# Kernel optimization log

Measured on AMD Instinct MI355X. Metric: run time of the kernel, lower is better.

The kernel has to match this reference:

```python
import jax, jax.numpy as jnp
import numpy as np

# hyperparameters (from init_kwargs)
GAMMA = 2.0
KEEP_WEIGHT = 1.0
T_TEMP = 0.07
M = 0.5
COS_M = float(np.cos(M))
SIN_M = float(np.sin(M))
THRESHOLD = float(np.cos(np.pi - M))
MM = float(np.sin(np.pi - M) * M)
ALPHA = 0.1
T_BUF0 = 0.0  # registered buffer t initialized to zero
VALID_THRESHOLD = 0.8
EPS = 1e-12  # F.normalize eps


def setup_inputs() -> dict:
    key = jax.random.key(0)
    k1, k2, k3 = jax.random.split(key, 3)
    N, C = 8192, 128
    return {
        "feature1": jax.random.normal(k1, (N, C), jnp.float32),
        "feature2": jax.random.normal(k2, (N, C), jnp.float32),
        "labels": jax.random.randint(k3, (N,), 0, 1024, dtype=jnp.int32),
    }


def reference(feature1, feature2, labels):
    N = feature1.shape[0]
    f1 = feature1 / jnp.maximum(jnp.linalg.norm(feature1, axis=1, keepdims=True), EPS)
    f2 = feature2 / jnp.maximum(jnp.linalg.norm(feature2, axis=1, keepdims=True), EPS)

    # [N, N] similarity, clamped to [-1, 1]
    sim = jnp.clip(jnp.einsum('nc,kc->nk', f1, f2), -1.0, 1.0)

    pos = (labels[:, None] == labels[None, :]).astype(sim.dtype)  # [N, N]
    neg = 1.0 - pos
    pos_mask = pos > 0

    # buffer update t (no_grad in original)
    mean_ts = jax.lax.stop_gradient((sim * pos).sum() / pos.sum())
    t = ALPHA * mean_ts + (1.0 - ALPHA) * T_BUF0
    weight_valid = t > VALID_THRESHOLD

    # curricular margin on positive entries
    sin_theta = jnp.sqrt(1.0 - sim * sim)
    cos_theta_m = sim * COS_M - sin_theta * SIN_M
    final_pos = jnp.where(sim > THRESHOLD, cos_theta_m, sim - MM)
    sim2 = jnp.where(pos_mask, final_pos, sim)

    # per-row mean of (margined) positive similarities
    row_target = (sim2 * pos).sum(axis=1) / pos.sum(axis=1)  # [N]
    hard_mask = sim2 > row_target[:, None]
    sim3 = jnp.where(hard_mask, sim2 * (t + sim2), sim2)
    sim4 = jnp.where(pos_mask, final_pos, sim3)

    logits = jnp.exp(sim4 / T_TEMP)

    # focal-style reweighting (only used when weight_valid)
    diff_pos = (pos - sim * pos) ** GAMMA + KEEP_WEIGHT * pos
    diff_neg = jnp.clip(sim * neg, 0.0, 1.0) ** GAMMA + KEEP_WEIGHT * neg

    logit_pos = jnp.where(weight_valid, (logits * diff_pos).sum(axis=1), (logits * pos).sum(axis=1))
    logit_neg = jnp.where(weight_valid, (logits * diff_neg).sum(axis=1), (logits * neg).sum(axis=1))

    loss = -jnp.log(logit_pos / (logit_neg + logit_pos)).sum() / N
    return loss
```

## Files before the change

kernel.cpp:

```cpp
#include <hip/hip_runtime.h>

#define N_ROWS 8192
#define N_LBL  1024
#define KMAX   64

constexpr float C_COS_M  = (float)0.8775825618903728;
constexpr float C_SIN_M  = (float)0.479425538604203;
constexpr float C_THRESH = (float)-0.8775825618903728;
constexpr float C_MM     = (float)0.2397127693021015;
constexpr float C_ALPHA  = 0.1f;
constexpr float C_VALID  = 0.8f;
constexpr float C_K2E    = (float)(1.0 / (0.07 * 0.6931471805599453));
constexpr float C_LN2    = 0.6931471805599453f;

typedef short s16x8 __attribute__((ext_vector_type(8)));
typedef float f32x4 __attribute__((ext_vector_type(4)));

__device__ __forceinline__ unsigned f2bf(float f) {
    unsigned u = __float_as_uint(f);
    return (u + 0x7fffu + ((u >> 16) & 1u)) >> 16;
}
__device__ __forceinline__ float bflo(unsigned u) { return __uint_as_float(u << 16); }
__device__ __forceinline__ float bfhi(unsigned u) { return __uint_as_float(u & 0xffff0000u); }

__device__ __forceinline__ void gl_lds16(const unsigned* g, void* lds) {
    __builtin_amdgcn_global_load_lds(
        (const __attribute__((address_space(1))) unsigned*)g,
        (__attribute__((address_space(3))) unsigned*)lds, 16, 0, 0);
}

__global__ void k_norm(const float* __restrict__ f1, const float* __restrict__ f2,
                       const int* __restrict__ labels,
                       unsigned* __restrict__ f1n, unsigned* __restrict__ f2n,
                       int* __restrict__ hist, unsigned short* __restrict__ bucket,
                       float* __restrict__ out) {
    if (blockIdx.x == 0 && threadIdx.x == 0) out[0] = 0.f;
    int b = blockIdx.x * 4 + (threadIdx.x >> 6);
    int l = threadIdx.x & 63;
    int row = (b < N_ROWS) ? b : (b - N_ROWS);
    const float* src = (b < N_ROWS) ? f1 : f2;
    unsigned* dst = (b < N_ROWS) ? f1n : f2n;
    float2 v = ((const float2*)(src + row * 128))[l];
    float ss = v.x * v.x + v.y * v.y;
    #pragma unroll
    for (int k = 1; k < 64; k <<= 1) ss += __shfl_xor(ss, k);
    float inv = 1.0f / fmaxf(sqrtf(ss), 1e-12f);
    dst[row * 64 + l] = f2bf(v.x * inv) | (f2bf(v.y * inv) << 16);
    if (b < N_ROWS && l == 0) {
        int lab = labels[row];
        int p = atomicAdd(&hist[lab], 1);
        if (p < KMAX) bucket[lab * KMAX + p] = (unsigned short)row;
    }
}

__global__ __launch_bounds__(256) void k_passA(const unsigned* __restrict__ f1n,
                                               const unsigned* __restrict__ f2n,
                                               const int* __restrict__ labels,
                                               const int* __restrict__ hist,
                                               const unsigned short* __restrict__ bucket,
                                               float* __restrict__ rt,
                                               float* __restrict__ row_sim,
                                               int* __restrict__ rowcnt,
                                               float* __restrict__ simlist) {
    int tid = threadIdx.x;
    int lane = tid & 63;
    int i = blockIdx.x * 4 + (tid >> 6);
    int g = lane >> 4, sl = lane & 15;
    uint4 a = ((const uint4*)(f1n + i * 64))[sl];
    float a0 = bflo(a.x), a1 = bfhi(a.x), a2 = bflo(a.y), a3 = bfhi(a.y);
    float a4 = bflo(a.z), a5 = bfhi(a.z), a6 = bflo(a.w), a7 = bfhi(a.w);
    int lab = labels[i];
    int cnt = hist[lab];
    int cntc = cnt < KMAX ? cnt : KMAX;
    float rs_sim = 0.f, rs_fp = 0.f;
    for (int e0 = 0; e0 < cntc; e0 += 4) {
        int e = e0 + g;
        bool val = e < cntc;
        int j = bucket[lab * KMAX + (val ? e : 0)];
        uint4 b = ((const uint4*)(f2n + j * 64))[sl];
        float p = a0 * bflo(b.x) + a1 * bfhi(b.x) + a2 * bflo(b.y) + a3 * bfhi(b.y)
                + a4 * bflo(b.z) + a5 * bfhi(b.z) + a6 * bflo(b.w) + a7 * bfhi(b.w);
        p += __shfl_xor(p, 1);
        p += __shfl_xor(p, 2);
        p += __shfl_xor(p, 4);
        p += __shfl_xor(p, 8);
        float s = fminf(1.f, fmaxf(-1.f, p));
        float ctm = s * C_COS_M - sqrtf(fmaxf(0.f, 1.f - s * s)) * C_SIN_M;
        float fpv = (s > C_THRESH) ? ctm : (s - C_MM);
        if (val) {
            rs_sim += s;
            rs_fp += fpv;
            if (sl == 0) simlist[i * KMAX + e] = s;
        }
    }
    rs_sim += __shfl_xor(rs_sim, 16); rs_sim += __shfl_xor(rs_sim, 32);
    rs_fp  += __shfl_xor(rs_fp, 16);  rs_fp  += __shfl_xor(rs_fp, 32);
    if (lane == 0) {
        rt[i] = rs_fp / (float)cnt;
        row_sim[i] = rs_sim;
        rowcnt[i] = cnt;
    }
}

__global__ void k_finalize(const float* __restrict__ row_sim, const int* __restrict__ hist,
                           float* __restrict__ tw) {
    int t = threadIdx.x;
    float ssum = 0.f, scnt = 0.f;
    if (t < N_LBL) { float h = (float)hist[t]; scnt = h * h; }
    #pragma unroll
    for (int p = 0; p < 8; ++p) ssum += row_sim[p * 1024 + t];
    #pragma unroll
    for (int k = 1; k < 64; k <<= 1) {
        ssum += __shfl_xor(ssum, k);
        scnt += __shfl_xor(scnt, k);
    }
    __shared__ float sa[16], sb[16];
    if ((t & 63) == 0) { sa[t >> 6] = ssum; sb[t >> 6] = scnt; }
    __syncthreads();
    if (t == 0) {
        float s1 = 0.f, s2 = 0.f;
        #pragma unroll
        for (int w = 0; w < 16; ++w) { s1 += sa[w]; s2 += sb[w]; }
        tw[0] = C_ALPHA * s1 / s2;
    }
}

#define MFMA_(A, B, C) __builtin_amdgcn_mfma_f32_16x16x32_bf16((A), (B), (C), 0, 0, 0)

#define STAGE_B(ct_) gl_lds16(gBsrc + (ct_) * 1024,                        \
                              ldsAll + 32768 + (((ct_) & 1) << 13) + wave * 1024)

#define LOADBF(ct_) { const unsigned char* pb_ =                           \
        ldsAll + 32768 + (((ct_) & 1) << 13) + bcol * 256;                 \
    bf0 = *((const s16x8*)(pb_ + (((0 * 4 + quad) ^ l15) << 4)));          \
    bf1 = *((const s16x8*)(pb_ + (((1 * 4 + quad) ^ l15) << 4)));          \
    bf2 = *((const s16x8*)(pb_ + (((2 * 4 + quad) ^ l15) << 4)));          \
    bf3 = *((const s16x8*)(pb_ + (((3 * 4 + quad) ^ l15) << 4))); }

#define EPI1(sv, rtvv, lnpv, WVC) {                                        \
    float s_ = (sv);                                                       \
    float u_ = C_K2E * s_;                                                 \
    float arg_ = (s_ > (rtvv)) ? u_ * (tval + s_) : u_;                    \
    float e_ = __builtin_amdgcn_exp2f(arg_);                               \
    if (WVC) { float cz_ = fmaxf(s_, 0.f); e_ = e_ * (cz_ * cz_ + 1.f); }  \
    (lnpv) += e_; }

#define TILE(WVC) {                                                        \
    f32x4 a0_ = (f32x4){0.f, 0.f, 0.f, 0.f};                               \
    f32x4 a1_ = (f32x4){0.f, 0.f, 0.f, 0.f};                               \
    a0_ = MFMA_(af00, bf0, a0_); a1_ = MFMA_(af10, bf0, a1_);              \
    a0_ = MFMA_(af01, bf1, a0_); a1_ = MFMA_(af11, bf1, a1_);              \
    a0_ = MFMA_(af02, bf2, a0_); a1_ = MFMA_(af12, bf2, a1_);              \
    a0_ = MFMA_(af03, bf3, a0_); a1_ = MFMA_(af13, bf3, a1_);              \
    EPI1(a0_[0], rtv00, lnp00, WVC); EPI1(a0_[1], rtv01, lnp01, WVC);      \
    EPI1(a0_[2], rtv02, lnp02, WVC); EPI1(a0_[3], rtv03, lnp03, WVC);      \
    EPI1(a1_[0], rtv10, lnp10, WVC); EPI1(a1_[1], rtv11, lnp11, WVC);      \
    EPI1(a1_[2], rtv12, lnp12, WVC); EPI1(a1_[3], rtv13, lnp13, WVC); }

#define RUNLOOP(WVC) {                                                     \
    _Pragma("unroll 1")                                                    \
    for (int ct = 0; ct < 16; ++ct) {                                      \
        if (ct) __syncthreads();                                           \
        if (ct + 1 < 16) STAGE_B(ct + 1);                                  \
        s16x8 bf0, bf1, bf2, bf3;                                          \
        LOADBF(ct);                                                        \
        TILE(WVC);                                                         \
    } }

#define STORE1(lnpv, mt, r) { float v_ = (lnpv);                           \
    v_ += __shfl_xor(v_, 1); v_ += __shfl_xor(v_, 2);                      \
    v_ += __shfl_xor(v_, 4); v_ += __shfl_xor(v_, 8);                      \
    if (l15 == 0)                                                          \
        lnacc2[slice * N_ROWS + rowbase + wr * 32 + (mt) * 16 + quad * 4 + (r)] = v_; }

__global__ __launch_bounds__(512, 4) void k_passB(const unsigned* __restrict__ f1n,
                                                  const unsigned* __restrict__ f2n,
                                                  const float* __restrict__ rt,
                                                  const float* __restrict__ tw,
                                                  float* __restrict__ lnacc2) {
    __shared__ __align__(16) unsigned char ldsAll[49152];
    const int tid = threadIdx.x;
    const int wave = tid >> 6, lane = tid & 63;
    const int wr = wave >> 1, wc = wave & 1;
    const int quad = lane >> 4, l15 = lane & 15;
    const int rowbase = blockIdx.x * 128;
    const float tval = tw[0];
    const bool wv = (tval > C_VALID);

    {
        const int srow = tid >> 4;
        const int sq   = (tid & 15) ^ (srow & 15);
        const unsigned* gA = f1n + rowbase * 64 + srow * 64 + sq * 4;
        const int loff = wave * 1024;
        #pragma unroll
        for (int it = 0; it < 4; ++it)
            gl_lds16(gA + it * 2048, ldsAll + loff + it * 8192);
    }

    const int col16 = tid >> 4;
    const int ch    = tid & 15;
    const unsigned* gBsrc = f2n
        + (blockIdx.y * 512 + ((col16 >> 4) << 8) + (col16 & 15)) * 64
        + ((ch ^ (col16 & 15)) << 2);

    STAGE_B(0);

    const int rbase = rowbase + wr * 32 + quad * 4;
    float rtv00 = rt[rbase + 0],  rtv01 = rt[rbase + 1];
    float rtv02 = rt[rbase + 2],  rtv03 = rt[rbase + 3];
    float rtv10 = rt[rbase + 16], rtv11 = rt[rbase + 17];
    float rtv12 = rt[rbase + 18], rtv13 = rt[rbase + 19];

    __syncthreads();

    const unsigned char* pA0 = ldsAll + (wr * 32 + l15) * 256;
    const unsigned char* pA1 = pA0 + 16 * 256;
    s16x8 af00 = *((const s16x8*)(pA0 + (((0 * 4 + quad) ^ l15) << 4)));
    s16x8 af01 = *((const s16x8*)(pA0 + (((1 * 4 + quad) ^ l15) << 4)));
    s16x8 af02 = *((const s16x8*)(pA0 + (((2 * 4 + quad) ^ l15) << 4)));
    s16x8 af03 = *((const s16x8*)(pA0 + (((3 * 4 + quad) ^ l15) << 4)));
    s16x8 af10 = *((const s16x8*)(pA1 + (((0 * 4 + quad) ^ l15) << 4)));
    s16x8 af11 = *((const s16x8*)(pA1 + (((1 * 4 + quad) ^ l15) << 4)));
    s16x8 af12 = *((const s16x8*)(pA1 + (((2 * 4 + quad) ^ l15) << 4)));
    s16x8 af13 = *((const s16x8*)(pA1 + (((3 * 4 + quad) ^ l15) << 4)));

    const int bcol = wc * 16 + l15;

    float lnp00 = 0.f, lnp01 = 0.f, lnp02 = 0.f, lnp03 = 0.f;
    float lnp10 = 0.f, lnp11 = 0.f, lnp12 = 0.f, lnp13 = 0.f;

    if (wv) { RUNLOOP(1); } else { RUNLOOP(0); }

    const int slice = blockIdx.y * 2 + wc;
    STORE1(lnp00, 0, 0); STORE1(lnp01, 0, 1); STORE1(lnp02, 0, 2); STORE1(lnp03, 0, 3);
    STORE1(lnp10, 1, 0); STORE1(lnp11, 1, 1); STORE1(lnp12, 1, 2); STORE1(lnp13, 1, 3);
}

__global__ void k_lossC(const float* __restrict__ simlist, const int* __restrict__ rowcnt,
                        const float* __restrict__ rt, const float* __restrict__ tw,
                        const float* __restrict__ lnacc2, float* __restrict__ out) {
    int t = threadIdx.x;
    int sub = t >> 3, sl = t & 7;
    int i = blockIdx.x * 32 + sub;
    int cnt = rowcnt[i];
    if (cnt > KMAX) cnt = KMAX;
    float tval = tw[0];
    bool wv = (tval > C_VALID);
    float rti = rt[i];
    float lp = 0.f, den = 0.f;
    for (int e = sl; e < cnt; e += 8) {
        float s = simlist[i * KMAX + e];
        float sh = (s > rti) ? s * (tval + s) : s;
        float en = __builtin_amdgcn_exp2f(C_K2E * sh);
        float ctm = s * C_COS_M - sqrtf(fmaxf(0.f, 1.f - s * s)) * C_SIN_M;
        float fp = (s > C_THRESH) ? ctm : (s - C_MM);
        float ep = __builtin_amdgcn_exp2f(C_K2E * fp);
        if (wv) {
            float cz = fmaxf(s, 0.f);
            en *= cz * cz + 1.f;
            float d = 1.f - s;
            ep *= d * d + 1.f;
        }
        den -= en;
        lp += ep;
    }
    float lnsum = 0.f;
    #pragma unroll
    for (int p = 0; p < 4; ++p) lnsum += lnacc2[(sl + p * 8) * N_ROWS + i];
    #pragma unroll
    for (int k = 1; k < 8; k <<= 1) {
        den += __shfl_xor(den, k);
        lp += __shfl_xor(lp, k);
        lnsum += __shfl_xor(lnsum, k);
    }
    float ln = lnsum + den;
    float rl = (__builtin_amdgcn_logf(lp + ln) - __builtin_amdgcn_logf(lp)) * C_LN2;
    rl += __shfl_xor(rl, 8);
    rl += __shfl_xor(rl, 16);
    rl += __shfl_xor(rl, 32);
    __shared__ float sa[4];
    if ((t & 63) == 0) sa[t >> 6] = rl;
    __syncthreads();
    if (t == 0)
        atomicAdd(out, (sa[0] + sa[1] + sa[2] + sa[3]) * (1.0f / (float)N_ROWS));
}

extern "C" void kernel_launch(void* const* d_in, const int* in_sizes, int n_in,
                              void* d_out, int out_size, void* d_ws, size_t ws_size,
                              hipStream_t stream) {
    (void)in_sizes; (void)n_in; (void)out_size; (void)ws_size;
    const float* f1 = (const float*)d_in[0];
    const float* f2 = (const float*)d_in[1];
    const int* labels = (const int*)d_in[2];
    float* out = (float*)d_out;
    char* ws = (char*)d_ws;

    unsigned* f1n          = (unsigned*)(ws + 0);
    unsigned* f2n          = (unsigned*)(ws + 2097152);
    float* simlist         = (float*)(ws + 4194304);
    float* rt              = (float*)(ws + 6291456);
    float* row_sim         = (float*)(ws + 6324224);
    int* rowcnt            = (int*)(ws + 6356992);
    float* lnacc2          = (float*)(ws + 6389760);
    unsigned short* bucket = (unsigned short*)(ws + 7438336);
    float* tw              = (float*)(ws + 7569408);
    int* hist              = (int*)(ws + 7569472);

    hipMemsetAsync(hist, 0, 4096, stream);

    k_norm<<<dim3(4096), dim3(256), 0, stream>>>(f1, f2, labels, f1n, f2n, hist, bucket, out);
    k_passA<<<dim3(2048), dim3(256), 0, stream>>>(f1n, f2n, labels, hist, bucket,
                                                  rt, row_sim, rowcnt, simlist);
    k_finalize<<<dim3(1), dim3(1024), 0, stream>>>(row_sim, hist, tw);
    k_passB<<<dim3(64, 16), dim3(512), 0, stream>>>(f1n, f2n, rt, tw, lnacc2);
    k_lossC<<<dim3(256), dim3(256), 0, stream>>>(simlist, rowcnt, rt, tw, lnacc2, out);
}
```

Measured before the change: 109.8 us.

## Load B fragments directly from global into registers, removing LDS staging and barriers

```diff
diff --git a/kernel.cpp b/kernel.cpp
--- a/kernel.cpp
+++ b/kernel.cpp
@@ -127,15 +127,15 @@
 
 #define MFMA_(A, B, C) __builtin_amdgcn_mfma_f32_16x16x32_bf16((A), (B), (C), 0, 0, 0)
 
-#define STAGE_B(ct_) gl_lds16(gBsrc + (ct_) * 1024,                        \
-                              ldsAll + 32768 + (((ct_) & 1) << 13) + wave * 1024)
-
-#define LOADBF(ct_) { const unsigned char* pb_ =                           \
-        ldsAll + 32768 + (((ct_) & 1) << 13) + bcol * 256;                 \
-    bf0 = *((const s16x8*)(pb_ + (((0 * 4 + quad) ^ l15) << 4)));          \
-    bf1 = *((const s16x8*)(pb_ + (((1 * 4 + quad) ^ l15) << 4)));          \
-    bf2 = *((const s16x8*)(pb_ + (((2 * 4 + quad) ^ l15) << 4)));          \
-    bf3 = *((const s16x8*)(pb_ + (((3 * 4 + quad) ^ l15) << 4))); }
+#define LD16(dst, addr, OFF) \
+    asm volatile("global_load_dwordx4 %0, %1, off offset:" #OFF : "=v"(dst) : "v"(addr))
+
+#define LOADASM(bp, ct_) { const unsigned* p_ = bb + (ct_) * 1024;         \
+    LD16(bp##0, p_, 0); LD16(bp##1, p_, 64);                               \
+    LD16(bp##2, p_, 128); LD16(bp##3, p_, 192); }
+
+#define WAITV(n_) asm volatile("s_waitcnt vmcnt(" #n_ ")" ::: "memory")
+#define SBAR      __builtin_amdgcn_sched_barrier(0)
 
 #define EPI1(sv, rtvv, lnpv, WVC) {                                        \
     float s_ = (sv);                                                       \
@@ -145,13 +145,13 @@
     if (WVC) { float cz_ = fmaxf(s_, 0.f); e_ = e_ * (cz_ * cz_ + 1.f); }  \
     (lnpv) += e_; }
 
-#define TILE(WVC) {                                                        \
+#define TILE(bp, WVC) {                                                    \
     f32x4 a0_ = (f32x4){0.f, 0.f, 0.f, 0.f};                               \
     f32x4 a1_ = (f32x4){0.f, 0.f, 0.f, 0.f};                               \
-    a0_ = MFMA_(af00, bf0, a0_); a1_ = MFMA_(af10, bf0, a1_);              \
-    a0_ = MFMA_(af01, bf1, a0_); a1_ = MFMA_(af11, bf1, a1_);              \
-    a0_ = MFMA_(af02, bf2, a0_); a1_ = MFMA_(af12, bf2, a1_);              \
-    a0_ = MFMA_(af03, bf3, a0_); a1_ = MFMA_(af13, bf3, a1_);              \
+    a0_ = MFMA_(af00, bp##0, a0_); a1_ = MFMA_(af10, bp##0, a1_);          \
+    a0_ = MFMA_(af01, bp##1, a0_); a1_ = MFMA_(af11, bp##1, a1_);          \
+    a0_ = MFMA_(af02, bp##2, a0_); a1_ = MFMA_(af12, bp##2, a1_);          \
+    a0_ = MFMA_(af03, bp##3, a0_); a1_ = MFMA_(af13, bp##3, a1_);          \
     EPI1(a0_[0], rtv00, lnp00, WVC); EPI1(a0_[1], rtv01, lnp01, WVC);      \
     EPI1(a0_[2], rtv02, lnp02, WVC); EPI1(a0_[3], rtv03, lnp03, WVC);      \
     EPI1(a1_[0], rtv10, lnp10, WVC); EPI1(a1_[1], rtv11, lnp11, WVC);      \
@@ -159,12 +159,14 @@
 
 #define RUNLOOP(WVC) {                                                     \
     _Pragma("unroll 1")                                                    \
-    for (int ct = 0; ct < 16; ++ct) {                                      \
-        if (ct) __syncthreads();                                           \
-        if (ct + 1 < 16) STAGE_B(ct + 1);                                  \
-        s16x8 bf0, bf1, bf2, bf3;                                          \
-        LOADBF(ct);                                                        \
-        TILE(WVC);                                                         \
+    for (int ct = 0; ct < 16; ct += 2) {                                   \
+        LOADASM(b1_, ct + 1);                                              \
+        WAITV(4); SBAR;                                                    \
+        TILE(b0_, WVC);                                                    \
+        if (ct + 2 < 16) { LOADASM(b0_, ct + 2); WAITV(4); }               \
+        else             { WAITV(0); }                                     \
+        SBAR;                                                              \
+        TILE(b1_, WVC);                                                    \
     } }
 
 #define STORE1(lnpv, mt, r) { float v_ = (lnpv);                           \
@@ -178,7 +180,7 @@
                                                   const float* __restrict__ rt,
                                                   const float* __restrict__ tw,
                                                   float* __restrict__ lnacc2) {
-    __shared__ __align__(16) unsigned char ldsAll[49152];
+    __shared__ __align__(16) unsigned char ldsA[32768];
     const int tid = threadIdx.x;
     const int wave = tid >> 6, lane = tid & 63;
     const int wr = wave >> 1, wc = wave & 1;
@@ -194,16 +196,14 @@
         const int loff = wave * 1024;
         #pragma unroll
         for (int it = 0; it < 4; ++it)
-            gl_lds16(gA + it * 2048, ldsAll + loff + it * 8192);
-    }
-
-    const int col16 = tid >> 4;
-    const int ch    = tid & 15;
-    const unsigned* gBsrc = f2n
-        + (blockIdx.y * 512 + ((col16 >> 4) << 8) + (col16 & 15)) * 64
-        + ((ch ^ (col16 & 15)) << 2);
-
-    STAGE_B(0);
+            gl_lds16(gA + it * 2048, ldsA + loff + it * 8192);
+    }
+
+    const unsigned* bb = f2n + (blockIdx.y * 512 + wc * 256 + l15) * 64 + quad * 4;
+
+    s16x8 b0_0, b0_1, b0_2, b0_3;
+    s16x8 b1_0, b1_1, b1_2, b1_3;
+    LOADASM(b0_, 0);
 
     const int rbase = rowbase + wr * 32 + quad * 4;
     float rtv00 = rt[rbase + 0],  rtv01 = rt[rbase + 1];
@@ -213,7 +213,7 @@
 
     __syncthreads();
 
-    const unsigned char* pA0 = ldsAll + (wr * 32 + l15) * 256;
+    const unsigned char* pA0 = ldsA + (wr * 32 + l15) * 256;
     const unsigned char* pA1 = pA0 + 16 * 256;
     s16x8 af00 = *((const s16x8*)(pA0 + (((0 * 4 + quad) ^ l15) << 4)));
     s16x8 af01 = *((const s16x8*)(pA0 + (((1 * 4 + quad) ^ l15) << 4)));
@@ -223,8 +223,6 @@
     s16x8 af11 = *((const s16x8*)(pA1 + (((1 * 4 + quad) ^ l15) << 4)));
     s16x8 af12 = *((const s16x8*)(pA1 + (((2 * 4 + quad) ^ l15) << 4)));
     s16x8 af13 = *((const s16x8*)(pA1 + (((3 * 4 + quad) ^ l15) << 4)));
-
-    const int bcol = wc * 16 + l15;
 
     float lnp00 = 0.f, lnp01 = 0.f, lnp02 = 0.f, lnp03 = 0.f;
     float lnp10 = 0.f, lnp11 = 0.f, lnp12 = 0.f, lnp13 = 0.f;
```

Result: slower. 144.3 us (+31.3%).

## Triple-buffer B tiles with vmcnt waits and fully unrolled two-tile phases

Applied to the files above, without the earlier changes.

```diff
diff --git a/kernel.cpp b/kernel.cpp
--- a/kernel.cpp
+++ b/kernel.cpp
@@ -127,58 +127,70 @@
 
 #define MFMA_(A, B, C) __builtin_amdgcn_mfma_f32_16x16x32_bf16((A), (B), (C), 0, 0, 0)
 
-#define STAGE_B(ct_) gl_lds16(gBsrc + (ct_) * 1024,                        \
-                              ldsAll + 32768 + (((ct_) & 1) << 13) + wave * 1024)
-
-#define LOADBF(ct_) { const unsigned char* pb_ =                           \
-        ldsAll + 32768 + (((ct_) & 1) << 13) + bcol * 256;                 \
-    bf0 = *((const s16x8*)(pb_ + (((0 * 4 + quad) ^ l15) << 4)));          \
-    bf1 = *((const s16x8*)(pb_ + (((1 * 4 + quad) ^ l15) << 4)));          \
-    bf2 = *((const s16x8*)(pb_ + (((2 * 4 + quad) ^ l15) << 4)));          \
+#define WAITV(n_) asm volatile("s_waitcnt vmcnt(" #n_ ")" ::: "memory")
+
+#define STAGE2(pp_, bf_) {                                                  \
+    gl_lds16(gBsrc + (pp_) * 2048,                                          \
+             ldsAll + 32768 + (bf_) * 16384 + wave * 1024);                 \
+    gl_lds16(gBsrc + (pp_) * 2048 + 1024,                                   \
+             ldsAll + 32768 + (bf_) * 16384 + 8192 + wave * 1024); }
+
+#define LOADBF(bf_, j_) { const unsigned char* pb_ =                        \
+        ldsAll + 32768 + (bf_) * 16384 + (j_) * 8192 + bcol * 256;          \
+    bf0 = *((const s16x8*)(pb_ + (((0 * 4 + quad) ^ l15) << 4)));           \
+    bf1 = *((const s16x8*)(pb_ + (((1 * 4 + quad) ^ l15) << 4)));           \
+    bf2 = *((const s16x8*)(pb_ + (((2 * 4 + quad) ^ l15) << 4)));           \
     bf3 = *((const s16x8*)(pb_ + (((3 * 4 + quad) ^ l15) << 4))); }
 
-#define EPI1(sv, rtvv, lnpv, WVC) {                                        \
-    float s_ = (sv);                                                       \
-    float u_ = C_K2E * s_;                                                 \
-    float arg_ = (s_ > (rtvv)) ? u_ * (tval + s_) : u_;                    \
-    float e_ = __builtin_amdgcn_exp2f(arg_);                               \
-    if (WVC) { float cz_ = fmaxf(s_, 0.f); e_ = e_ * (cz_ * cz_ + 1.f); }  \
+#define EPI1(sv, rtvv, lnpv, WVC) {                                         \
+    float s_ = (sv);                                                        \
+    float u_ = C_K2E * s_;                                                  \
+    float arg_ = (s_ > (rtvv)) ? u_ * (tval + s_) : u_;                     \
+    float e_ = __builtin_amdgcn_exp2f(arg_);                                \
+    if (WVC) { float cz_ = fmaxf(s_, 0.f); e_ = e_ * (cz_ * cz_ + 1.f); }   \
     (lnpv) += e_; }
 
-#define TILE(WVC) {                                                        \
-    f32x4 a0_ = (f32x4){0.f, 0.f, 0.f, 0.f};                               \
-    f32x4 a1_ = (f32x4){0.f, 0.f, 0.f, 0.f};                               \
-    a0_ = MFMA_(af00, bf0, a0_); a1_ = MFMA_(af10, bf0, a1_);              \
-    a0_ = MFMA_(af01, bf1, a0_); a1_ = MFMA_(af11, bf1, a1_);              \
-    a0_ = MFMA_(af02, bf2, a0_); a1_ = MFMA_(af12, bf2, a1_);              \
-    a0_ = MFMA_(af03, bf3, a0_); a1_ = MFMA_(af13, bf3, a1_);              \
-    EPI1(a0_[0], rtv00, lnp00, WVC); EPI1(a0_[1], rtv01, lnp01, WVC);      \
-    EPI1(a0_[2], rtv02, lnp02, WVC); EPI1(a0_[3], rtv03, lnp03, WVC);      \
-    EPI1(a1_[0], rtv10, lnp10, WVC); EPI1(a1_[1], rtv11, lnp11, WVC);      \
+#define TILE(WVC) {                                                         \
+    f32x4 a0_ = (f32x4){0.f, 0.f, 0.f, 0.f};                                \
+    f32x4 a1_ = (f32x4){0.f, 0.f, 0.f, 0.f};                                \
+    a0_ = MFMA_(af00, bf0, a0_); a1_ = MFMA_(af10, bf0, a1_);               \
+    a0_ = MFMA_(af01, bf1, a0_); a1_ = MFMA_(af11, bf1, a1_);               \
+    a0_ = MFMA_(af02, bf2, a0_); a1_ = MFMA_(af12, bf2, a1_);               \
+    a0_ = MFMA_(af03, bf3, a0_); a1_ = MFMA_(af13, bf3, a1_);               \
+    EPI1(a0_[0], rtv00, lnp00, WVC); EPI1(a0_[1], rtv01, lnp01, WVC);       \
+    EPI1(a0_[2], rtv02, lnp02, WVC); EPI1(a0_[3], rtv03, lnp03, WVC);       \
+    EPI1(a1_[0], rtv10, lnp10, WVC); EPI1(a1_[1], rtv11, lnp11, WVC);       \
     EPI1(a1_[2], rtv12, lnp12, WVC); EPI1(a1_[3], rtv13, lnp13, WVC); }
 
-#define RUNLOOP(WVC) {                                                     \
-    _Pragma("unroll 1")                                                    \
-    for (int ct = 0; ct < 16; ++ct) {                                      \
-        if (ct) __syncthreads();                                           \
-        if (ct + 1 < 16) STAGE_B(ct + 1);                                  \
-        s16x8 bf0, bf1, bf2, bf3;                                          \
-        LOADBF(ct);                                                        \
-        TILE(WVC);                                                         \
-    } }
-
-#define STORE1(lnpv, mt, r) { float v_ = (lnpv);                           \
-    v_ += __shfl_xor(v_, 1); v_ += __shfl_xor(v_, 2);                      \
-    v_ += __shfl_xor(v_, 4); v_ += __shfl_xor(v_, 8);                      \
-    if (l15 == 0)                                                          \
+#define PH(pp_, bf_, wn_, dostage_, sbf_, WVC) {                            \
+    WAITV(wn_);                                                             \
+    __builtin_amdgcn_s_barrier();                                           \
+    if (dostage_) STAGE2((pp_) + 2, sbf_);                                  \
+    { s16x8 bf0, bf1, bf2, bf3; LOADBF(bf_, 0); TILE(WVC); }                \
+    { s16x8 bf0, bf1, bf2, bf3; LOADBF(bf_, 1); TILE(WVC); } }
+
+#define RUNLOOP(WVC) {                                                      \
+    PH(0, 0, 2, 1, 2, WVC)                                                  \
+    PH(1, 1, 2, 1, 0, WVC)                                                  \
+    PH(2, 2, 2, 1, 1, WVC)                                                  \
+    PH(3, 0, 2, 1, 2, WVC)                                                  \
+    PH(4, 1, 2, 1, 0, WVC)                                                  \
+    PH(5, 2, 2, 1, 1, WVC)                                                  \
+    PH(6, 0, 2, 0, 0, WVC)                                                  \
+    PH(7, 1, 0, 0, 0, WVC) }
+
+#define STORE1(lnpv, mt, r) { float v_ = (lnpv);                            \
+    v_ += __shfl_xor(v_, 1); v_ += __shfl_xor(v_, 2);                       \
+    v_ += __shfl_xor(v_, 4); v_ += __shfl_xor(v_, 8);                       \
+    if (l15 == 0)                                                           \
         lnacc2[slice * N_ROWS + rowbase + wr * 32 + (mt) * 16 + quad * 4 + (r)] = v_; }
 
-__global__ __launch_bounds__(512, 4) void k_passB(const unsigned* __restrict__ f1n,
-                                                  const unsigned* __restrict__ f2n,
-                                                  const float* __restrict__ rt,
-                                                  const float* __restrict__ tw,
-                                                  float* __restrict__ lnacc2) {
-    __shared__ __align__(16) unsigned char ldsAll[49152];
+__global__ __launch_bounds__(512) void k_passB(const unsigned* __restrict__ f1n,
+                                               const unsigned* __restrict__ f2n,
+                                               const float* __restrict__ rt,
+                                               const float* __restrict__ tw,
+                                               float* __restrict__ lnacc2) {
+    __shared__ __align__(16) unsigned char ldsAll[81920];
     const int tid = threadIdx.x;
     const int wave = tid >> 6, lane = tid & 63;
     const int wr = wave >> 1, wc = wave & 1;
@@ -203,7 +215,8 @@
         + (blockIdx.y * 512 + ((col16 >> 4) << 8) + (col16 & 15)) * 64
         + ((ch ^ (col16 & 15)) << 2);
 
-    STAGE_B(0);
+    STAGE2(0, 0);
+    STAGE2(1, 1);
 
     const int rbase = rowbase + wr * 32 + quad * 4;
     float rtv00 = rt[rbase + 0],  rtv01 = rt[rbase + 1];
```

New measurement: 114.8 us. +4.5%, slower.
